# Optimization experiments

Hardware: AMD Instinct MI355X
Metric: run time of the kernel (lower is better)

## Reference

```python
import jax, jax.numpy as jnp
import numpy as np

EPS = 1e-4
GX, GY, ZMAX = 512, 512, 64
S0 = (GX, GY, ZMAX)

# ---------- rulebook construction (numpy, setup-time only) ----------

def _lin(c, S):
    return (c[:, 0].astype(np.int64) * S[1] + c[:, 1]) * S[2] + c[:, 2]

def _lookup(skeys, order, qk):
    pos = np.searchsorted(skeys, qk)
    pc = np.clip(pos, 0, len(skeys) - 1)
    ok = skeys[pc] == qk
    return np.where(ok, order[pc], -1).astype(np.int32)

def _sm_rulebook(coords, S):
    # submanifold 3x3x3: for each active site, index of neighbor at each of 27 offsets (-1 if inactive)
    keys = _lin(coords, S)
    order = np.argsort(keys).astype(np.int64); skeys = keys[order]
    Sa = np.array(S)
    cols = []
    for d in [(i, j, k) for i in (-1, 0, 1) for j in (-1, 0, 1) for k in (-1, 0, 1)]:
        q = coords + np.array(d)
        inb = np.all((q >= 0) & (q < Sa), axis=1)
        nb = _lookup(skeys, order, _lin(np.clip(q, 0, None), S))
        cols.append(np.where(inb, nb, -1).astype(np.int32))
    return np.stack(cols, 1)  # [N, 27]

def _down_rulebook(coords, S):
    # strided 2x2x2 conv: coarse sites = unique(coords//2); [Nc, 8] child indices into fine level
    Sc = (S[0] // 2, S[1] // 2, S[2] // 2)
    pk = np.unique(_lin(coords // 2, Sc))
    z = pk % Sc[2]; y = (pk // Sc[2]) % Sc[1]; x = pk // (Sc[1] * Sc[2])
    pcoords = np.stack([x, y, z], 1)
    keys = _lin(coords, S)
    order = np.argsort(keys).astype(np.int64); skeys = keys[order]
    cols = []
    for d in [(i, j, k) for i in (0, 1) for j in (0, 1) for k in (0, 1)]:
        cols.append(_lookup(skeys, order, _lin(pcoords * 2 + np.array(d), S)))
    return np.stack(cols, 1), pcoords, Sc

def _coords0():
    # road-like 2.5D surface: one active voxel per (x, y) column -> exactly 512*512 unique sites
    xs, ys = np.meshgrid(np.arange(GX), np.arange(GY), indexing='ij')
    x = xs.ravel().astype(np.int64); y = ys.ravel().astype(np.int64)
    z = (32 + 8 * np.sin(x / 37.0) + 8 * np.cos(y / 53.0) + 3 * np.sin((x + y) / 17.0)).astype(np.int64)
    z = np.clip(z, 0, ZMAX - 1)
    return np.stack([x, y, z], 1)


def setup_inputs() -> dict:
    c0 = _coords0()
    nbr_0 = _sm_rulebook(c0, S0)
    rb_0, c1, S1 = _down_rulebook(c0, S0)
    nbr_1 = _sm_rulebook(c1, S1)
    rb_1, c2, S2 = _down_rulebook(c1, S1)
    nbr_2 = _sm_rulebook(c2, S2)

    key = jax.random.key(0)
    ks = iter(jax.random.split(key, 40))
    def w(shape):
        fan = float(np.prod(shape[:-1]))
        return (jax.random.normal(next(ks), shape, jnp.float32) / np.sqrt(fan)).astype(jnp.float32)
    def gb(c):  # row 0 = gamma (~1), row 1 = beta (~0)
        base = jnp.concatenate([jnp.ones((1, c), jnp.float32), jnp.zeros((1, c), jnp.float32)], 0)
        return base + 0.01 * jax.random.normal(next(ks), (2, c), jnp.float32)

    N0 = c0.shape[0]
    return dict(
        feat=jax.random.normal(next(ks), (N0, 3), jnp.float32),
        w_in=w((27, 3, 32)),
        bn1_0=gb(32), w_sm1_0=w((27, 32, 32)),
        bnd_0=gb(32), w_down_0=w((8, 32, 64)),
        bn1_1=gb(64), w_sm1_1=w((27, 64, 64)),
        bnd_1=gb(64), w_down_1=w((8, 64, 96)),
        bn1_2=gb(96), w_sm1_2=w((27, 96, 96)),
        bnu_1=gb(96), w_up_1=w((8, 96, 64)),
        bn2_1=gb(128), w_sm2_1=w((27, 128, 64)),
        bnu_0=gb(64), w_up_0=w((8, 64, 32)),
        bn2_0=gb(64), w_sm2_0=w((27, 64, 32)),
        bnf=gb(32),
        lin_w=w((32, 2)), lin_b=jnp.zeros((2,), jnp.float32),
        nbr_0=jnp.asarray(nbr_0), nbr_1=jnp.asarray(nbr_1), nbr_2=jnp.asarray(nbr_2),
        rb_0=jnp.asarray(rb_0), rb_1=jnp.asarray(rb_1),
    )

# ---------- jax forward ----------

def bn_relu(x, gb):
    # SCN BatchNormReLU: normalize over all active sites (biased var), affine, then ReLU
    mu = jnp.mean(x, 0)
    var = jnp.var(x, 0)
    return jax.nn.relu((x - mu) * (gb[0] / jnp.sqrt(var + EPS)) + gb[1])

def sm_conv(feat, nbr, W):
    # submanifold conv: gather 27 neighbors (zero for inactive), per-offset GEMM, accumulate
    out = jnp.zeros((feat.shape[0], W.shape[2]), feat.dtype)
    for k in range(W.shape[0]):
        idx = nbr[:, k]
        g = jnp.where((idx >= 0)[:, None], feat[jnp.clip(idx, 0)], 0.0)
        out = out + g @ W[k]
    return out

def down_conv(feat, rb, W):
    # strided 2x2x2 conv: gather children of each coarse site
    out = jnp.zeros((rb.shape[0], W.shape[2]), feat.dtype)
    for k in range(W.shape[0]):
        idx = rb[:, k]
        g = jnp.where((idx >= 0)[:, None], feat[jnp.clip(idx, 0)], 0.0)
        out = out + g @ W[k]
    return out

def up_conv(feat_c, rb, W, n_fine):
    # deconv (transpose of down_conv): scatter coarse features back to fine active sites
    out = jnp.zeros((n_fine, W.shape[2]), feat_c.dtype)
    for k in range(W.shape[0]):
        idx = rb[:, k]
        contrib = jnp.where((idx >= 0)[:, None], feat_c @ W[k], 0.0)
        out = out.at[jnp.clip(idx, 0)].add(contrib)
    return out


def reference(feat, w_in, bn1_0, w_sm1_0, bnd_0, w_down_0, bn1_1, w_sm1_1, bnd_1, w_down_1,
              bn1_2, w_sm1_2, bnu_1, w_up_1, bn2_1, w_sm2_1, bnu_0, w_up_0, bn2_0, w_sm2_0,
              bnf, lin_w, lin_b, nbr_0, nbr_1, nbr_2, rb_0, rb_1):
    x0 = sm_conv(feat, nbr_0, w_in)                              # initial SMConv 3 -> 32
    x0 = sm_conv(bn_relu(x0, bn1_0), nbr_0, w_sm1_0)             # level-0 entry block
    d0 = down_conv(bn_relu(x0, bnd_0), rb_0, w_down_0)           # [N1, 64]
    x1 = sm_conv(bn_relu(d0, bn1_1), nbr_1, w_sm1_1)             # level-1 entry block
    d1 = down_conv(bn_relu(x1, bnd_1), rb_1, w_down_1)           # [N2, 96]
    x2 = sm_conv(bn_relu(d1, bn1_2), nbr_2, w_sm1_2)             # innermost block
    u1 = up_conv(bn_relu(x2, bnu_1), rb_1, w_up_1, x1.shape[0])  # deconv 96 -> 64
    y1 = sm_conv(bn_relu(jnp.concatenate([x1, u1], 1), bn2_1), nbr_1, w_sm2_1)  # 128 -> 64
    u0 = up_conv(bn_relu(y1, bnu_0), rb_0, w_up_0, x0.shape[0])  # deconv 64 -> 32
    y0 = sm_conv(bn_relu(jnp.concatenate([x0, u0], 1), bn2_0), nbr_0, w_sm2_0)  # 64 -> 32
    out = bn_relu(y0, bnf)                                       # final BatchNormReLU(m)
    return out @ lin_w + lin_b                                   # Linear(m, 2)
```

## Files before the change

### kernel.cpp

```cpp
#include <hip/hip_runtime.h>
#include <hip/hip_bf16.h>


typedef __hip_bfloat16 hbf;
typedef __attribute__((ext_vector_type(8))) short short8;
typedef __attribute__((ext_vector_type(4))) float f32x4;
typedef const __attribute__((address_space(1))) short gas_short;
typedef __attribute__((address_space(3))) short las_short;

__device__ inline float b2f(short s) {
    unsigned u = ((unsigned)(unsigned short)s) << 16;
    float f; __builtin_memcpy(&f, &u, 4); return f;
}
__device__ inline short f2b(float f) {
    hbf h = __float2bfloat16(f);
    short s; __builtin_memcpy(&s, &h, 2); return s;
}

struct WPA {
    const float* src[9];
    short* dst[9];
    int CI[9], CO[9];
    int cum[10];
};
__global__ __launch_bounds__(256) void wprep_all(WPA a, int total) {
    int e0 = blockIdx.x * 256 + threadIdx.x;
    if (e0 >= total) return;
    int L = 0;
#pragma unroll
    for (int i = 1; i < 9; i++) L += (e0 >= a.cum[i]) ? 1 : 0;
    int e = e0 - a.cum[L];
    int CI = a.CI[L], CO = a.CO[L];
    int NT = CO >> 4, NCH = CI >> 5;
    int j    = e & 7;
    int lane = (e >> 3) & 63;
    int t    = (e >> 9) % NT;
    int c    = (e / (512 * NT)) % NCH;
    int k    = e / (512 * NT * NCH);
    int ci = c * 32 + (lane >> 4) * 8 + j;
    int co = t * 16 + (lane & 15);
    a.dst[L][e] = f2b(a.src[L][((long long)k * CI + ci) * CO + co]);
}

__global__ void zerok(float* p, int n) {
    int i = blockIdx.x * 256 + threadIdx.x;
    if (i < n) p[i] = 0.f;
}

__global__ __launch_bounds__(256) void nbrmask_k(const int* __restrict__ nbr,
                                                 unsigned* __restrict__ msk, int N) {
    long long r = (long long)blockIdx.x * 256 + threadIdx.x;
    if (r >= N) return;
    unsigned mv = 0;
#pragma unroll
    for (int k = 0; k < 27; k++)
        mv |= (nbr[r * 27 + k] >= 0) ? (1u << k) : 0u;
    msk[r] = mv;
}

__global__ __launch_bounds__(256) void conv_in(
    const float* __restrict__ feat, const int* __restrict__ nbr,
    const float* __restrict__ W, short* __restrict__ out, int N) {
    __shared__ float sW[27 * 96];
    const int tid = threadIdx.x;
    for (int e = tid; e < 27 * 96; e += 256) sW[e] = W[e];
    __syncthreads();
    long long r = (long long)blockIdx.x * 256 + tid;
    if (r >= N) return;
    float acc[32];
#pragma unroll
    for (int c = 0; c < 32; c++) acc[c] = 0.f;
    for (int k = 0; k < 27; k++) {
        int idx = nbr[r * 27 + k];
        if (idx >= 0) {
            float f0 = feat[(long long)idx * 3];
            float f1 = feat[(long long)idx * 3 + 1];
            float f2 = feat[(long long)idx * 3 + 2];
            const float* w = sW + k * 96;
#pragma unroll
            for (int c = 0; c < 32; c++)
                acc[c] += f0 * w[c] + f1 * w[32 + c] + f2 * w[64 + c];
        }
    }
#pragma unroll
    for (int c = 0; c < 32; c++) out[r * 32 + c] = f2b(acc[c]);
}

template<int CI1, int CI2, int COUT>
__global__ __launch_bounds__(256) void stencil0(
    const short* __restrict__ fA, const short* __restrict__ fB,
    const unsigned* __restrict__ msk, const short* __restrict__ Wf,
    short* __restrict__ out, float* __restrict__ pstat,
    const float* __restrict__ abA, const float* __restrict__ abB, int N) {
    constexpr int CIT  = CI1 + CI2;
    constexpr int NCH  = CIT / 32;
    constexpr int NT   = COUT / 16;
    constexpr int MT   = 2;
    constexpr int CIB  = CIT * 2;
    constexpr int ROWS = 130;
    constexpr int NC8  = CIT / 8;
    constexpr int SWB  = (CIB >= 128) ? 7 : 3;
    __shared__ __attribute__((aligned(16))) char sA[3 * ROWS * CIB];
    const int tid  = threadIdx.x;
    const int lane = tid & 63;
    const int wid  = tid >> 6;
    const int m    = lane & 15;
    const int quad = lane >> 4;
    const int bid  = blockIdx.x;
    const int xq     = bid >> 2;
    const int ystart = (bid & 3) << 7;
    const long long R = (long long)bid * 128;

    {
        const int c8 = tid % NC8;
        const bool isA = (c8 * 8) < CI1;
        const short* src  = isA ? fA : fB;
        const float* abp  = isA ? abA : abB;
        const int   srcCI = isA ? CI1 : CI2;
        const int   chb   = isA ? c8 * 8 : c8 * 8 - CI1;
        float s_[8], b_[8];
#pragma unroll
        for (int jj = 0; jj < 8; jj++) {
            s_[jj] = abp[chb + jj];
            b_[jj] = abp[srcCI + chb + jj];
        }
        for (int e = tid; e < 3 * ROWS * NC8; e += 256) {
            int rr = (e / NC8) % ROWS;
            int st = e / (NC8 * ROWS);
            long long gr = (long long)(xq - 1 + st) * 512 + (ystart - 1 + rr);
            long long grc = (gr < 0 || gr >= N) ? 0 : gr;
            short8 v = *reinterpret_cast<const short8*>(src + grc * srcCI + chb);
            short8 o;
#pragma unroll
            for (int jj = 0; jj < 8; jj++) {
                float f = b2f(v[jj]) * s_[jj] + b_[jj];
                o[jj] = f2b(f > 0.f ? f : 0.f);
            }
            int byte = (st * ROWS + rr) * CIB + c8 * 16;
            byte ^= ((rr & SWB) << 4);
            *reinterpret_cast<short8*>(sA + byte) = o;
        }
    }
    __syncthreads();

    f32x4 acc[MT][NT];
#pragma unroll
    for (int mt = 0; mt < MT; mt++)
#pragma unroll
        for (int t = 0; t < NT; t++) acc[mt][t] = (f32x4)0.f;

    unsigned mv[MT];
#pragma unroll
    for (int mt = 0; mt < MT; mt++) {
        long long r = R + wid * 32 + mt * 16 + m;
        mv[mt] = (r < N) ? msk[r] : 0u;
    }

#pragma unroll
    for (int s9 = 0; s9 < 9; s9++) {
        const int st = s9 / 3;
        const int dy = s9 % 3 - 1;
        short8 a[MT][NCH];
#pragma unroll
        for (int mt = 0; mt < MT; mt++) {
            int rl = 1 + wid * 32 + mt * 16 + m + dy;
#pragma unroll
            for (int c = 0; c < NCH; c++) {
                int byte = (st * ROWS + rl) * CIB + (c * 4 + quad) * 16;
                byte ^= ((rl & SWB) << 4);
                a[mt][c] = *reinterpret_cast<const short8*>(sA + byte);
            }
        }
#pragma unroll
        for (int z3 = 0; z3 < 3; z3++) {
            const int k = s9 * 3 + z3;
            unsigned anyb = (mv[0] >> k) & 1;
            if (MT > 1) anyb |= (mv[1] >> k) & 1;
            if (__any(anyb)) {
                short8 bf[NCH][NT];
#pragma unroll
                for (int c = 0; c < NCH; c++)
#pragma unroll
                    for (int t = 0; t < NT; t++)
                        bf[c][t] = *reinterpret_cast<const short8*>(
                            Wf + ((size_t)(k * NCH + c) * NT + t) * 512 + lane * 8);
#pragma unroll
                for (int mt = 0; mt < MT; mt++) {
                    const bool bb = (mv[mt] >> k) & 1;
                    short8 asel[NCH];
#pragma unroll
                    for (int c = 0; c < NCH; c++)
                        asel[c] = bb ? a[mt][c] : (short8)0;
#pragma unroll
                    for (int c = 0; c < NCH; c++)
#pragma unroll
                        for (int t = 0; t < NT; t++)
                            acc[mt][t] = __builtin_amdgcn_mfma_f32_16x16x32_bf16(
                                asel[c], bf[c][t], acc[mt][t], 0, 0, 0);
                }
            }
        }
    }

    float s[NT], q[NT];
#pragma unroll
    for (int t = 0; t < NT; t++) { s[t] = 0.f; q[t] = 0.f; }
#pragma unroll
    for (int mt = 0; mt < MT; mt++) {
#pragma unroll
        for (int g4 = 0; g4 < 4; g4++) {
            long long sr = R + wid * 32 + mt * 16 + quad * 4 + g4;
            if (sr < N) {
#pragma unroll
                for (int t = 0; t < NT; t++) {
                    float v = acc[mt][t][g4];
                    out[sr * COUT + t * 16 + m] = f2b(v);
                    s[t] += v; q[t] += v * v;
                }
            }
        }
    }
    float* pb = pstat + (blockIdx.x & 7) * 2 * COUT;
#pragma unroll
    for (int t = 0; t < NT; t++) {
        float sv = s[t], qv = q[t];
        sv += __shfl_xor(sv, 16); qv += __shfl_xor(qv, 16);
        sv += __shfl_xor(sv, 32); qv += __shfl_xor(qv, 32);
        if (quad == 0) {
            atomicAdd(&pb[t * 16 + m], sv);
            atomicAdd(&pb[COUT + t * 16 + m], qv);
        }
    }
}

template<int CI1, int CI2, int COUT, int K, int G, int MT, bool FACT>
__global__ __launch_bounds__(256) void gmfma10(
    const short* __restrict__ fA, const short* __restrict__ fB,
    const int* __restrict__ nbr, const short* __restrict__ Wf,
    short* __restrict__ out, float* __restrict__ pstat,
    const float* __restrict__ abp, int N) {
    static_assert(K % G == 0, "G must divide K");
    static_assert(!FACT || CI2 == 0, "fused act only for single input");
    constexpr int NT  = COUT / 16;
    constexpr int NC1 = CI1 / 32;
    constexpr int NC2 = CI2 / 32;
    constexpr int NCH = (CI1 + CI2) / 32;
    constexpr int PANEL = NCH * NT * 512;
    constexpr int GSH   = G * PANEL;
    constexpr int NPH   = K / G;
    constexpr int WCH   = GSH / 4;
    constexpr int S16   = (WCH * 2) / 1024;
    constexpr int S4    = ((WCH * 2) % 1024) / 256;
    __shared__ __attribute__((aligned(16))) short sB[GSH];
    const int tid  = threadIdx.x;
    const int lane = tid & 63;
    const int wid  = tid >> 6;
    const int m    = lane & 15;
    const int quad = lane >> 4;
    const long long tb0 = ((long long)blockIdx.x * 4 + wid) * (MT * 16);

    f32x4 acc[MT][NT];
#pragma unroll
    for (int mt = 0; mt < MT; mt++)
#pragma unroll
        for (int t = 0; t < NT; t++) acc[mt][t] = (f32x4)0.f;

#define STAGE(ph)                                                              \
    {                                                                          \
        const short* _src = Wf + (size_t)(ph) * GSH + wid * WCH;               \
        short* _dst = &sB[wid * WCH];                                          \
        _Pragma("unroll")                                                      \
        for (int i = 0; i < S16; i++)                                          \
            __builtin_amdgcn_global_load_lds(                                  \
                (gas_short*)(_src + i * 512 + lane * 8),                       \
                (las_short*)(_dst + i * 512), 16, 0, 0);                       \
        _Pragma("unroll")                                                      \
        for (int i = 0; i < S4; i++)                                           \
            __builtin_amdgcn_global_load_lds(                                  \
                (gas_short*)(_src + S16 * 512 + i * 128 + lane * 2),           \
                (las_short*)(_dst + S16 * 512 + i * 128), 4, 0, 0);            \
    }

    STAGE(0)
    __builtin_amdgcn_sched_barrier(0);

    int idxs[MT][K];
#pragma unroll
    for (int mt = 0; mt < MT; mt++) {
        long long r = tb0 + mt * 16 + m;
        bool rv = r < N;
#pragma unroll
        for (int k = 0; k < K; k++)
            idxs[mt][k] = rv ? nbr[r * K + k] : -1;
    }
    unsigned pmask[MT];
#pragma unroll
    for (int mt = 0; mt < MT; mt++) {
        unsigned pm = 0;
#pragma unroll
        for (int k = 0; k < K; k++)
            pm |= __any(idxs[mt][k] >= 0) ? (1u << k) : 0u;
        pmask[mt] = __builtin_amdgcn_readfirstlane(pm);
    }

    float aS[FACT ? NC1 * 8 : 1], aBb[FACT ? NC1 * 8 : 1];
    if constexpr (FACT) {
#pragma unroll
        for (int c = 0; c < NC1; c++)
#pragma unroll
            for (int jj = 0; jj < 8; jj++) {
                int ch = c * 32 + quad * 8 + jj;
                aS[c * 8 + jj]  = abp[ch];
                aBb[c * 8 + jj] = abp[CI1 + ch];
            }
    }

    __builtin_amdgcn_sched_barrier(0);
    asm volatile("s_waitcnt vmcnt(0)" ::: "memory");
    __builtin_amdgcn_s_barrier();
    __builtin_amdgcn_sched_barrier(0);
    asm volatile("" ::: "memory");

    short8 S[3][NCH];

#define LOADS(sl, mt, kk)                                                      \
    {                                                                          \
        int _i = idxs[mt][kk];                                                 \
        long long _j = _i < 0 ? 0 : _i;                                        \
        _Pragma("unroll")                                                      \
        for (int c = 0; c < NC1; c++) {                                        \
            short8 _v = *reinterpret_cast<const short8*>(                      \
                fA + _j * CI1 + c * 32 + quad * 8);                            \
            if constexpr (FACT) {                                              \
                short8 _o;                                                     \
                _Pragma("unroll")                                              \
                for (int jj = 0; jj < 8; jj++) {                               \
                    float _f = b2f(_v[jj]) * aS[c * 8 + jj] + aBb[c * 8 + jj]; \
                    _o[jj] = f2b(_f > 0.f ? _f : 0.f);                         \
                }                                                              \
                _v = _o;                                                       \
            }                                                                  \
            S[sl][c] = (_i >= 0) ? _v : (short8)0;                             \
        }                                                                      \
        if constexpr (NC2 > 0) {                                               \
            _Pragma("unroll")                                                  \
            for (int c = 0; c < NC2; c++) {                                    \
                short8 _v = *reinterpret_cast<const short8*>(                  \
                    fB + _j * CI2 + c * 32 + quad * 8);                        \
                S[sl][NC1 + c] = (_i >= 0) ? _v : (short8)0;                   \
            }                                                                  \
        }                                                                      \
    }
#define MFMAS(sl, mt, jl)                                                      \
    {                                                                          \
        _Pragma("unroll")                                                      \
        for (int c = 0; c < NCH; c++) {                                        \
            _Pragma("unroll")                                                  \
            for (int t = 0; t < NT; t++) {                                     \
                short8 b = *reinterpret_cast<const short8*>(                   \
                    &sB[((jl) * NCH * NT + c * NT + t) * 512 + lane * 8]);     \
                acc[mt][t] = __builtin_amdgcn_mfma_f32_16x16x32_bf16(          \
                    S[sl][c], b, acc[mt][t], 0, 0, 0);                         \
            }                                                                  \
        }                                                                      \
    }

#pragma unroll
    for (int ph = 0; ph < NPH; ph++) {
#pragma unroll
        for (int mt = 0; mt < MT; mt++) {
            const unsigned mm = (pmask[mt] >> (ph * G)) & ((1u << G) - 1);
#pragma unroll
            for (int j = 0; j < G + 2; j++) {
                if (j < G)
                    if (mm & (1u << j)) LOADS(j % 3, mt, ph * G + j)
                if (j >= 2)
                    if (mm & (1u << (j - 2))) MFMAS((j - 2) % 3, mt, j - 2)
            }
        }
        if (ph + 1 < NPH) {
            __builtin_amdgcn_sched_barrier(0);
            asm volatile("s_waitcnt lgkmcnt(0)" ::: "memory");
            __builtin_amdgcn_s_barrier();
            __builtin_amdgcn_sched_barrier(0);
            STAGE(ph + 1)
            __builtin_amdgcn_sched_barrier(0);
            asm volatile("s_waitcnt vmcnt(0)" ::: "memory");
            __builtin_amdgcn_s_barrier();
            __builtin_amdgcn_sched_barrier(0);
            asm volatile("" ::: "memory");
        }
    }
#undef LOADS
#undef MFMAS
#undef STAGE
    float s[NT], q[NT];
#pragma unroll
    for (int t = 0; t < NT; t++) { s[t] = 0.f; q[t] = 0.f; }
#pragma unroll
    for (int mt = 0; mt < MT; mt++) {
#pragma unroll
        for (int g4 = 0; g4 < 4; g4++) {
            long long sr = tb0 + mt * 16 + quad * 4 + g4;
            if (sr < N) {
#pragma unroll
                for (int t = 0; t < NT; t++) {
                    float v = acc[mt][t][g4];
                    out[sr * COUT + t * 16 + m] = f2b(v);
                    s[t] += v; q[t] += v * v;
                }
            }
        }
    }
    float* pb = pstat + (blockIdx.x & 7) * 2 * COUT;
#pragma unroll
    for (int t = 0; t < NT; t++) {
        float sv = s[t], qv = q[t];
        sv += __shfl_xor(sv, 16); qv += __shfl_xor(qv, 16);
        sv += __shfl_xor(sv, 32); qv += __shfl_xor(qv, 32);
        if (quad == 0) {
            atomicAdd(&pb[t * 16 + m], sv);
            atomicAdd(&pb[COUT + t * 16 + m], qv);
        }
    }
}

template<int CIN, int COUT, int G>
__global__ __launch_bounds__(256) void upmfma10(
    const short* __restrict__ f, const int* __restrict__ rb,
    const short* __restrict__ Wf, short* __restrict__ out,
    float* __restrict__ pstat, const float* __restrict__ abp, int N) {
    static_assert(8 % G == 0, "G must divide 8");
    constexpr int NT = COUT / 16;
    constexpr int NK = CIN / 32;
    constexpr int PANEL = NK * NT * 512;
    constexpr int GSH   = G * PANEL;
    constexpr int NPH   = 8 / G;
    constexpr int WCH   = GSH / 4;
    constexpr int S16   = (WCH * 2) / 1024;
    constexpr int S4    = ((WCH * 2) % 1024) / 256;
    __shared__ __attribute__((aligned(16))) short sB[GSH];
    const int tid  = threadIdx.x;
    const int lane = tid & 63;
    const int wid  = tid >> 6;
    const int m    = lane & 15;
    const int quad = lane >> 4;
    const long long row0 = ((long long)blockIdx.x * 4 + wid) * 16;
    const long long r = row0 + m;
    const bool rv = r < N;
    const long long rc = rv ? r : 0;

#define STAGE(ph)                                                              \
    {                                                                          \
        const short* _src = Wf + (size_t)(ph) * GSH + wid * WCH;               \
        short* _dst = &sB[wid * WCH];                                          \
        _Pragma("unroll")                                                      \
        for (int i = 0; i < S16; i++)                                          \
            __builtin_amdgcn_global_load_lds(                                  \
                (gas_short*)(_src + i * 512 + lane * 8),                       \
                (las_short*)(_dst + i * 512), 16, 0, 0);                       \
        _Pragma("unroll")                                                      \
        for (int i = 0; i < S4; i++)                                           \
            __builtin_amdgcn_global_load_lds(                                  \
                (gas_short*)(_src + S16 * 512 + i * 128 + lane * 2),           \
                (las_short*)(_dst + S16 * 512 + i * 128), 4, 0, 0);            \
    }
    STAGE(0)
    __builtin_amdgcn_sched_barrier(0);

    short8 af[NK];
#pragma unroll
    for (int kc = 0; kc < NK; kc++) {
        short8 v = *reinterpret_cast<const short8*>(
            f + rc * CIN + kc * 32 + quad * 8);
        short8 o;
#pragma unroll
        for (int jj = 0; jj < 8; jj++) {
            int ch = kc * 32 + quad * 8 + jj;
            float u = b2f(v[jj]) * abp[ch] + abp[CIN + ch];
            o[jj] = f2b(u > 0.f ? u : 0.f);
        }
        af[kc] = rv ? o : (short8)0;
    }
    int sidx[8][4];
#pragma unroll
    for (int g4 = 0; g4 < 4; g4++) {
        long long sr = row0 + quad * 4 + g4;
#pragma unroll
        for (int k = 0; k < 8; k++)
            sidx[k][g4] = (sr < N) ? rb[sr * 8 + k] : -1;
    }
    unsigned pm = 0;
#pragma unroll
    for (int k = 0; k < 8; k++) {
        int anyv = (sidx[k][0] >= 0) | (sidx[k][1] >= 0) |
                   (sidx[k][2] >= 0) | (sidx[k][3] >= 0);
        pm |= __any(anyv) ? (1u << k) : 0u;
    }
    pm = __builtin_amdgcn_readfirstlane(pm);

    float s[NT], q[NT];
#pragma unroll
    for (int t = 0; t < NT; t++) { s[t] = 0.f; q[t] = 0.f; }

    __builtin_amdgcn_sched_barrier(0);
    asm volatile("s_waitcnt vmcnt(0)" ::: "memory");
    __builtin_amdgcn_s_barrier();
    __builtin_amdgcn_sched_barrier(0);
    asm volatile("" ::: "memory");

#pragma unroll
    for (int ph = 0; ph < NPH; ph++) {
#pragma unroll
        for (int j = 0; j < G; j++) {
            const int k = ph * G + j;
            if (pm & (1u << k)) {
                f32x4 acc[NT];
#pragma unroll
                for (int t = 0; t < NT; t++) acc[t] = (f32x4)0.f;
#pragma unroll
                for (int kc = 0; kc < NK; kc++) {
#pragma unroll
                    for (int t = 0; t < NT; t++) {
                        short8 b = *reinterpret_cast<const short8*>(
                            &sB[(j * NK * NT + kc * NT + t) * 512 + lane * 8]);
                        acc[t] = __builtin_amdgcn_mfma_f32_16x16x32_bf16(
                            af[kc], b, acc[t], 0, 0, 0);
                    }
                }
#pragma unroll
                for (int g4 = 0; g4 < 4; g4++) {
                    if (sidx[k][g4] >= 0) {
#pragma unroll
                        for (int t = 0; t < NT; t++) {
                            float v = acc[t][g4];
                            out[(long long)sidx[k][g4] * COUT + t * 16 + m] =
                                f2b(v);
                            s[t] += v; q[t] += v * v;
                        }
                    }
                }
            }
        }
        if (ph + 1 < NPH) {
            __builtin_amdgcn_sched_barrier(0);
            asm volatile("s_waitcnt lgkmcnt(0)" ::: "memory");
            __builtin_amdgcn_s_barrier();
            __builtin_amdgcn_sched_barrier(0);
            STAGE(ph + 1)
            __builtin_amdgcn_sched_barrier(0);
            asm volatile("s_waitcnt vmcnt(0)" ::: "memory");
            __builtin_amdgcn_s_barrier();
            __builtin_amdgcn_sched_barrier(0);
            asm volatile("" ::: "memory");
        }
    }
#undef STAGE
    float* pb = pstat + (blockIdx.x & 7) * 2 * COUT;
#pragma unroll
    for (int t = 0; t < NT; t++) {
        float sv = s[t], qv = q[t];
        sv += __shfl_xor(sv, 16); qv += __shfl_xor(qv, 16);
        sv += __shfl_xor(sv, 32); qv += __shfl_xor(qv, 32);
        if (quad == 0) {
            atomicAdd(&pb[t * 16 + m], sv);
            atomicAdd(&pb[COUT + t * 16 + m], qv);
        }
    }
}

template<int C>
__global__ void bn_stats(const short* __restrict__ x, double* __restrict__ part, int N) {
    constexpr int GR  = C / 8;
    constexpr int RPB = 256 / GR;
    constexpr int ACTIVE = GR * RPB;
    __shared__ double ls[256 * 8];
    __shared__ double lq[256 * 8];
    const int tid = threadIdx.x;
    const int g   = tid % GR;
    const int rr  = tid / GR;
    double s[8], q[8];
#pragma unroll
    for (int j = 0; j < 8; j++) { s[j] = 0.0; q[j] = 0.0; }
    if (tid < ACTIVE) {
        for (long long r = (long long)blockIdx.x * RPB + rr; r < N;
             r += (long long)gridDim.x * RPB) {
            short8 v = *reinterpret_cast<const short8*>(x + r * C + g * 8);
#pragma unroll
            for (int j = 0; j < 8; j++) {
                double f = (double)b2f(v[j]);
                s[j] += f; q[j] += f * f;
            }
        }
    }
#pragma unroll
    for (int j = 0; j < 8; j++) { ls[tid * 8 + j] = s[j]; lq[tid * 8 + j] = q[j]; }
    __syncthreads();
    if (tid < C) {
        int gg = tid / 8, jj = tid % 8;
        double S = 0.0, Q = 0.0;
        for (int r2 = 0; r2 < RPB; r2++) {
            S += ls[(r2 * GR + gg) * 8 + jj];
            Q += lq[(r2 * GR + gg) * 8 + jj];
        }
        part[blockIdx.x * 256 + tid]       = S;
        part[blockIdx.x * 256 + 128 + tid] = Q;
    }
}

__global__ void bn_fin(const double* __restrict__ part, const float* __restrict__ gb,
                       int gbfull, int goff, float* __restrict__ ab,
                       int C, int P, double invN) {
    __shared__ double ss[256], sq[256];
    const int tid = threadIdx.x;
    const int c   = tid % C;
    const int g   = tid / C;
    const int G   = 256 / C;
    double s = 0.0, q = 0.0;
    if (g < G) {
        for (int p = g; p < P; p += G) {
            s += part[p * 256 + c];
            q += part[p * 256 + 128 + c];
        }
    }
    ss[tid] = s; sq[tid] = q;
    __syncthreads();
    if (tid < C) {
        for (int j = 1; j < G; j++) { s += ss[j * C + c]; q += sq[j * C + c]; }
        double mu  = s * invN;
        double var = q * invN - mu * mu;
        double a   = (double)gb[goff + c] / sqrt(var + 1e-4);
        ab[c]     = (float)a;
        ab[C + c] = (float)((double)gb[gbfull + goff + c] - mu * a);
    }
}

__global__ void bn_fin_a(const float* __restrict__ pst, const float* __restrict__ gb,
                         int gbfull, int goff, float* __restrict__ ab,
                         int C, double invN) {
    int c = threadIdx.x;
    if (c >= C) return;
    double s = 0.0, q = 0.0;
#pragma unroll
    for (int b = 0; b < 8; b++) {
        s += (double)pst[b * 2 * C + c];
        q += (double)pst[b * 2 * C + C + c];
    }
    double mu  = s * invN;
    double var = q * invN - mu * mu;
    double a   = (double)gb[goff + c] / sqrt(var + 1e-4);
    ab[c]     = (float)a;
    ab[C + c] = (float)((double)gb[gbfull + goff + c] - mu * a);
}

template<int C>
__global__ void bnact(const short* __restrict__ x, const float* __restrict__ ab,
                      short* __restrict__ y, long long total8) {
    long long i = (long long)blockIdx.x * blockDim.x + threadIdx.x;
    if (i >= total8) return;
    long long base = i * 8;
    int c0 = (int)(base % C);
    short8 v = *reinterpret_cast<const short8*>(x + base);
    short8 o;
#pragma unroll
    for (int j = 0; j < 8; j++) {
        float f = b2f(v[j]) * ab[c0 + j] + ab[C + c0 + j];
        o[j] = f2b(f > 0.f ? f : 0.f);
    }
    *reinterpret_cast<short8*>(y + base) = o;
}

template<int C>
__global__ void bnact2(const short* __restrict__ xa, const float* __restrict__ aba,
                       short* __restrict__ ya,
                       const short* __restrict__ xb, const float* __restrict__ abb,
                       short* __restrict__ yb, long long n8) {
    long long i = (long long)blockIdx.x * blockDim.x + threadIdx.x;
    if (i >= 2 * n8) return;
    const short* x; const float* ab; short* y; long long ii;
    if (i < n8) { x = xa; ab = aba; y = ya; ii = i; }
    else        { x = xb; ab = abb; y = yb; ii = i - n8; }
    long long base = ii * 8;
    int c0 = (int)(base % C);
    short8 v = *reinterpret_cast<const short8*>(x + base);
    short8 o;
#pragma unroll
    for (int j = 0; j < 8; j++) {
        float f = b2f(v[j]) * ab[c0 + j] + ab[C + c0 + j];
        o[j] = f2b(f > 0.f ? f : 0.f);
    }
    *reinterpret_cast<short8*>(y + base) = o;
}

__global__ void final_k(const short* __restrict__ x, const float* __restrict__ ab,
                        const float* __restrict__ lw, const float* __restrict__ lb,
                        float* __restrict__ out, int N) {
    long long r = (long long)blockIdx.x * blockDim.x + threadIdx.x;
    if (r >= N) return;
    float a0 = lb[0], a1 = lb[1];
#pragma unroll
    for (int j = 0; j < 4; j++) {
        short8 v = *reinterpret_cast<const short8*>(x + r * 32 + j * 8);
#pragma unroll
        for (int t = 0; t < 8; t++) {
            int ci = 8 * j + t;
            float u = b2f(v[t]) * ab[ci] + ab[32 + ci];
            u = u > 0.f ? u : 0.f;
            a0 += u * lw[ci * 2];
            a1 += u * lw[ci * 2 + 1];
        }
    }
    out[2 * r]     = a0;
    out[2 * r + 1] = a1;
}

extern "C" void kernel_launch(void* const* d_in, const int* in_sizes, int n_in,
                              void* d_out, int out_size, void* d_ws, size_t ws_size,
                              hipStream_t stream) {
    const long long N0 = in_sizes[0] / 3;
    const long long N1 = in_sizes[26] / 8;
    const long long N2 = in_sizes[27] / 8;
    const int P = 256;

    const float* feat = (const float*)d_in[0];
    const int* nbr0 = (const int*)d_in[23];
    const int* nbr1 = (const int*)d_in[24];
    const int* nbr2 = (const int*)d_in[25];
    const int* rb0  = (const int*)d_in[26];
    const int* rb1  = (const int*)d_in[27];

    char* p = (char*)d_ws;
    double* part = (double*)p;            p += (size_t)P * 256 * 8;
    float*  ab   = (float*)p;             p += 12 * 256 * 4;
    float*  pst  = (float*)p;             p += (size_t)10 * 2048 * 4;
    unsigned* msk0 = (unsigned*)p;        p += ((size_t)N0 * 4 + 63) & ~(size_t)63;
    const int wLayer[9] = {3, 5, 7, 9, 11, 13, 15, 17, 19};
    const int wK[9]  = {27, 8, 27, 8, 27, 8, 27, 8, 27};
    const int wCI[9] = {32, 32, 64, 64, 96, 96, 128, 64, 64};
    const int wCO[9] = {32, 64, 64, 96, 96, 64, 64, 32, 32};
    short* wt[9];
    WPA wpa;
    int cum = 0;
    for (int i = 0; i < 9; i++) {
        wt[i] = (short*)p;
        int n = wK[i] * wCI[i] * wCO[i];
        p += (((size_t)n * 2 + 63) & ~(size_t)63);
        wpa.src[i] = (const float*)d_in[wLayer[i]];
        wpa.dst[i] = wt[i];
        wpa.CI[i] = wCI[i]; wpa.CO[i] = wCO[i];
        wpa.cum[i] = cum; cum += n;
    }
    wpa.cum[9] = cum;
    auto balloc = [&](long long elems) {
        short* q = (short*)p;
        p += (((size_t)elems * 2 + 63) & ~(size_t)63);
        return q;
    };
    short* R0 = balloc(N0 * 32);
    short* R1 = balloc(N0 * 32);
    short* R2 = balloc(N1 * 64);
    short* R3 = balloc(N0 * 32);
    short* Xb = balloc(N0 * 32);
    short* Yb = balloc(N0 * 32);

    wprep_all<<<(cum + 255) / 256, 256, 0, stream>>>(wpa, cum);
    zerok<<<(10 * 2048 + 255) / 256, 256, 0, stream>>>(pst, 10 * 2048);
    nbrmask_k<<<(int)((N0 + 255) / 256), 256, 0, stream>>>(nbr0, msk0, (int)N0);

#define AB(SL) (ab + (SL) * 256)
#define PS(SL) (pst + (SL) * 2048)
#define FINA(PSL, GBI, GBFULL, GOFF, SL, CH, NN)                                     \
    bn_fin_a<<<1, 128, 0, stream>>>(PS(PSL), (const float*)d_in[GBI], GBFULL, GOFF,  \
                                    AB(SL), CH, 1.0 / (double)(NN))
#define GB1(N_) (int)(((N_) + 63) / 64)
#define GB2(N_) (int)(((N_) + 127) / 128)

    conv_in<<<(int)((N0 + 255) / 256), 256, 0, stream>>>(
        feat, nbr0, (const float*)d_in[1], R0, (int)N0);
    bn_stats<32><<<P, 256, 0, stream>>>(R0, part, (int)N0);
    bn_fin<<<1, 256, 0, stream>>>(part, (const float*)d_in[2], 32, 0,
                                  AB(0), 32, P, 1.0 / (double)N0);
    stencil0<32, 0, 32><<<GB2(N0), 256, 0, stream>>>(
        R0, nullptr, msk0, wt[0], R1, PS(0), AB(0), nullptr, (int)N0);
    FINA(0, 4, 32, 0, 1, 32, N0);
    FINA(0, 18, 64, 0, 9, 32, N0);
    gmfma10<32, 0, 64, 8, 8, 2, true><<<GB2(N1), 256, 0, stream>>>(
        R1, nullptr, rb0, wt[1], R0, PS(1), AB(1), (int)N1);
    FINA(1, 6, 64, 0, 2, 64, N1);

    bnact<64><<<(int)((N1 * 64 / 8 + 255) / 256), 256, 0, stream>>>(
        R0, AB(2), Xb, N1 * 64 / 8);
    gmfma10<64, 0, 64, 27, 3, 2, false><<<GB2(N1), 256, 0, stream>>>(
        Xb, nullptr, nbr1, wt[2], R2, PS(2), nullptr, (int)N1);
    FINA(2, 8, 64, 0, 3, 64, N1);
    FINA(2, 14, 128, 0, 6, 64, N1);
    gmfma10<64, 0, 96, 8, 2, 1, true><<<GB1(N2), 256, 0, stream>>>(
        R2, nullptr, rb1, wt[3], R0, PS(3), AB(3), (int)N2);
    FINA(3, 10, 96, 0, 4, 96, N2);

    bnact<96><<<(int)((N2 * 96 / 8 + 255) / 256), 256, 0, stream>>>(
        R0, AB(4), Xb, N2 * 96 / 8);
    gmfma10<96, 0, 96, 27, 3, 1, false><<<GB1(N2), 256, 0, stream>>>(
        Xb, nullptr, nbr2, wt[4], R3, PS(4), nullptr, (int)N2);
    FINA(4, 12, 96, 0, 5, 96, N2);

    upmfma10<96, 64, 2><<<GB1(N2), 256, 0, stream>>>(
        R3, rb1, wt[5], R0, PS(5), AB(5), (int)N2);
    FINA(5, 14, 128, 64, 7, 64, N1);
    bnact2<64><<<(int)((2 * (N1 * 64 / 8) + 255) / 256), 256, 0, stream>>>(
        R2, AB(6), Xb, R0, AB(7), Yb, N1 * 64 / 8);
    gmfma10<64, 64, 64, 27, 3, 2, false><<<GB2(N1), 256, 0, stream>>>(
        Xb, Yb, nbr1, wt[6], R3, PS(6), nullptr, (int)N1);
    FINA(6, 16, 64, 0, 8, 64, N1);

    upmfma10<64, 32, 4><<<GB1(N1), 256, 0, stream>>>(
        R3, rb0, wt[7], R0, PS(7), AB(8), (int)N1);
    FINA(7, 18, 64, 32, 10, 32, N0);
    stencil0<32, 32, 32><<<GB2(N0), 256, 0, stream>>>(
        R1, R0, msk0, wt[8], R3, PS(8), AB(9), AB(10), (int)N0);
    FINA(8, 20, 32, 0, 11, 32, N0);

    final_k<<<(int)((N0 + 255) / 256), 256, 0, stream>>>(
        R3, AB(11), (const float*)d_in[21], (const float*)d_in[22],
        (float*)d_out, (int)N0);

#undef AB
#undef PS
#undef FINA
#undef GB1
#undef GB2
}
```

Before: 566.0 us.

## Read MFMA weight fragments directly from global memory instead of staging in LDS

The gathered-conv and up-conv MFMA kernels no longer stage weight panels into shared memory with async global-to-LDS loads and phase barriers. Each wave now loads its B fragments straight from global memory (relying on L1/L2 caching), and the phased loop becomes a single software-pipelined loop over all kernel offsets. This removes LDS usage, block-wide barriers and phase synchronisation, which may raise occupancy. The cost is redundant per-wave global/cache traffic for the weights and exposed load latency before each MFMA.

After: 681.5 us. 1.2x slower.

```diff
diff --git a/kernel.cpp b/kernel.cpp
--- a/kernel.cpp
+++ b/kernel.cpp
@@ -5,8 +5,6 @@
 typedef __hip_bfloat16 hbf;
 typedef __attribute__((ext_vector_type(8))) short short8;
 typedef __attribute__((ext_vector_type(4))) float f32x4;
-typedef const __attribute__((address_space(1))) short gas_short;
-typedef __attribute__((address_space(3))) short las_short;
 
 __device__ inline float b2f(short s) {
     unsigned u = ((unsigned)(unsigned short)s) << 16;
@@ -233,25 +231,17 @@
     }
 }
 
-template<int CI1, int CI2, int COUT, int K, int G, int MT, bool FACT>
-__global__ __launch_bounds__(256) void gmfma10(
+template<int CI1, int CI2, int COUT, int K, int MT, bool FACT>
+__global__ __launch_bounds__(256) void gmfma11(
     const short* __restrict__ fA, const short* __restrict__ fB,
     const int* __restrict__ nbr, const short* __restrict__ Wf,
     short* __restrict__ out, float* __restrict__ pstat,
     const float* __restrict__ abp, int N) {
-    static_assert(K % G == 0, "G must divide K");
     static_assert(!FACT || CI2 == 0, "fused act only for single input");
     constexpr int NT  = COUT / 16;
     constexpr int NC1 = CI1 / 32;
     constexpr int NC2 = CI2 / 32;
     constexpr int NCH = (CI1 + CI2) / 32;
-    constexpr int PANEL = NCH * NT * 512;
-    constexpr int GSH   = G * PANEL;
-    constexpr int NPH   = K / G;
-    constexpr int WCH   = GSH / 4;
-    constexpr int S16   = (WCH * 2) / 1024;
-    constexpr int S4    = ((WCH * 2) % 1024) / 256;
-    __shared__ __attribute__((aligned(16))) short sB[GSH];
     const int tid  = threadIdx.x;
     const int lane = tid & 63;
     const int wid  = tid >> 6;
@@ -265,25 +255,6 @@
 #pragma unroll
         for (int t = 0; t < NT; t++) acc[mt][t] = (f32x4)0.f;
 
-#define STAGE(ph)                                                              \
-    {                                                                          \
-        const short* _src = Wf + (size_t)(ph) * GSH + wid * WCH;               \
-        short* _dst = &sB[wid * WCH];                                          \
-        _Pragma("unroll")                                                      \
-        for (int i = 0; i < S16; i++)                                          \
-            __builtin_amdgcn_global_load_lds(                                  \
-                (gas_short*)(_src + i * 512 + lane * 8),                       \
-                (las_short*)(_dst + i * 512), 16, 0, 0);                       \
-        _Pragma("unroll")                                                      \
-        for (int i = 0; i < S4; i++)                                           \
-            __builtin_amdgcn_global_load_lds(                                  \
-                (gas_short*)(_src + S16 * 512 + i * 128 + lane * 2),           \
-                (las_short*)(_dst + S16 * 512 + i * 128), 4, 0, 0);            \
-    }
-
-    STAGE(0)
-    __builtin_amdgcn_sched_barrier(0);
-
     int idxs[MT][K];
 #pragma unroll
     for (int mt = 0; mt < MT; mt++) {
@@ -314,12 +285,6 @@
                 aBb[c * 8 + jj] = abp[CI1 + ch];
             }
     }
-
-    __builtin_amdgcn_sched_barrier(0);
-    asm volatile("s_waitcnt vmcnt(0)" ::: "memory");
-    __builtin_amdgcn_s_barrier();
-    __builtin_amdgcn_sched_barrier(0);
-    asm volatile("" ::: "memory");
 
     short8 S[3][NCH];
 
@@ -351,14 +316,14 @@
             }                                                                  \
         }                                                                      \
     }
-#define MFMAS(sl, mt, jl)                                                      \
+#define MFMAD(sl, mt, kk)                                                      \
     {                                                                          \
         _Pragma("unroll")                                                      \
         for (int c = 0; c < NCH; c++) {                                        \
             _Pragma("unroll")                                                  \
             for (int t = 0; t < NT; t++) {                                     \
                 short8 b = *reinterpret_cast<const short8*>(                   \
-                    &sB[((jl) * NCH * NT + c * NT + t) * 512 + lane * 8]);     \
+                    Wf + ((size_t)((kk) * NCH + c) * NT + t) * 512 + lane * 8);\
                 acc[mt][t] = __builtin_amdgcn_mfma_f32_16x16x32_bf16(          \
                     S[sl][c], b, acc[mt][t], 0, 0, 0);                         \
             }                                                                  \
@@ -366,34 +331,19 @@
     }
 
 #pragma unroll
-    for (int ph = 0; ph < NPH; ph++) {
-#pragma unroll
-        for (int mt = 0; mt < MT; mt++) {
-            const unsigned mm = (pmask[mt] >> (ph * G)) & ((1u << G) - 1);
-#pragma unroll
-            for (int j = 0; j < G + 2; j++) {
-                if (j < G)
-                    if (mm & (1u << j)) LOADS(j % 3, mt, ph * G + j)
-                if (j >= 2)
-                    if (mm & (1u << (j - 2))) MFMAS((j - 2) % 3, mt, j - 2)
-            }
-        }
-        if (ph + 1 < NPH) {
-            __builtin_amdgcn_sched_barrier(0);
-            asm volatile("s_waitcnt lgkmcnt(0)" ::: "memory");
-            __builtin_amdgcn_s_barrier();
-            __builtin_amdgcn_sched_barrier(0);
-            STAGE(ph + 1)
-            __builtin_amdgcn_sched_barrier(0);
-            asm volatile("s_waitcnt vmcnt(0)" ::: "memory");
-            __builtin_amdgcn_s_barrier();
-            __builtin_amdgcn_sched_barrier(0);
-            asm volatile("" ::: "memory");
+    for (int mt = 0; mt < MT; mt++) {
+        const unsigned mm = pmask[mt];
+        if (mm & 1u) LOADS(0, mt, 0)
+        if (K > 1 && (mm & 2u)) LOADS(1, mt, 1)
+#pragma unroll
+        for (int k = 0; k < K; k++) {
+            if (k + 2 < K)
+                if (mm & (1u << (k + 2))) LOADS((k + 2) % 3, mt, k + 2)
+            if (mm & (1u << k)) MFMAD(k % 3, mt, k)
         }
     }
 #undef LOADS
-#undef MFMAS
-#undef STAGE
+#undef MFMAD
     float s[NT], q[NT];
 #pragma unroll
     for (int t = 0; t < NT; t++) { s[t] = 0.f; q[t] = 0.f; }
@@ -425,21 +375,13 @@
     }
 }
 
-template<int CIN, int COUT, int G>
-__global__ __launch_bounds__(256) void upmfma10(
+template<int CIN, int COUT>
+__global__ __launch_bounds__(256) void upmfma11(
     const short* __restrict__ f, const int* __restrict__ rb,
     const short* __restrict__ Wf, short* __restrict__ out,
     float* __restrict__ pstat, const float* __restrict__ abp, int N) {
-    static_assert(8 % G == 0, "G must divide 8");
     constexpr int NT = COUT / 16;
     constexpr int NK = CIN / 32;
-    constexpr int PANEL = NK * NT * 512;
-    constexpr int GSH   = G * PANEL;
-    constexpr int NPH   = 8 / G;
-    constexpr int WCH   = GSH / 4;
-    constexpr int S16   = (WCH * 2) / 1024;
-    constexpr int S4    = ((WCH * 2) % 1024) / 256;
-    __shared__ __attribute__((aligned(16))) short sB[GSH];
     const int tid  = threadIdx.x;
     const int lane = tid & 63;
     const int wid  = tid >> 6;
@@ -450,24 +392,6 @@
     const bool rv = r < N;
     const long long rc = rv ? r : 0;
 
-#define STAGE(ph)                                                              \
-    {                                                                          \
-        const short* _src = Wf + (size_t)(ph) * GSH + wid * WCH;               \
-        short* _dst = &sB[wid * WCH];                                          \
-        _Pragma("unroll")                                                      \
-        for (int i = 0; i < S16; i++)                                          \
-            __builtin_amdgcn_global_load_lds(                                  \
-                (gas_short*)(_src + i * 512 + lane * 8),                       \
-                (las_short*)(_dst + i * 512), 16, 0, 0);                       \
-        _Pragma("unroll")                                                      \
-        for (int i = 0; i < S4; i++)                                           \
-            __builtin_amdgcn_global_load_lds(                                  \
-                (gas_short*)(_src + S16 * 512 + i * 128 + lane * 2),           \
-                (las_short*)(_dst + S16 * 512 + i * 128), 4, 0, 0);            \
-    }
-    STAGE(0)
-    __builtin_amdgcn_sched_barrier(0);
-
     short8 af[NK];
 #pragma unroll
     for (int kc = 0; kc < NK; kc++) {
@@ -503,59 +427,35 @@
 #pragma unroll
     for (int t = 0; t < NT; t++) { s[t] = 0.f; q[t] = 0.f; }
 
-    __builtin_amdgcn_sched_barrier(0);
-    asm volatile("s_waitcnt vmcnt(0)" ::: "memory");
-    __builtin_amdgcn_s_barrier();
-    __builtin_amdgcn_sched_barrier(0);
-    asm volatile("" ::: "memory");
-
-#pragma unroll
-    for (int ph = 0; ph < NPH; ph++) {
-#pragma unroll
-        for (int j = 0; j < G; j++) {
-            const int k = ph * G + j;
-            if (pm & (1u << k)) {
-                f32x4 acc[NT];
-#pragma unroll
-                for (int t = 0; t < NT; t++) acc[t] = (f32x4)0.f;
-#pragma unroll
-                for (int kc = 0; kc < NK; kc++) {
+#pragma unroll
+    for (int k = 0; k < 8; k++) {
+        if (pm & (1u << k)) {
+            f32x4 acc[NT];
+#pragma unroll
+            for (int t = 0; t < NT; t++) acc[t] = (f32x4)0.f;
+#pragma unroll
+            for (int kc = 0; kc < NK; kc++) {
+#pragma unroll
+                for (int t = 0; t < NT; t++) {
+                    short8 b = *reinterpret_cast<const short8*>(
+                        Wf + ((size_t)(k * NK + kc) * NT + t) * 512 + lane * 8);
+                    acc[t] = __builtin_amdgcn_mfma_f32_16x16x32_bf16(
+                        af[kc], b, acc[t], 0, 0, 0);
+                }
+            }
+#pragma unroll
+            for (int g4 = 0; g4 < 4; g4++) {
+                if (sidx[k][g4] >= 0) {
 #pragma unroll
                     for (int t = 0; t < NT; t++) {
-                        short8 b = *reinterpret_cast<const short8*>(
-                            &sB[(j * NK * NT + kc * NT + t) * 512 + lane * 8]);
-                        acc[t] = __builtin_amdgcn_mfma_f32_16x16x32_bf16(
-                            af[kc], b, acc[t], 0, 0, 0);
+                        float v = acc[t][g4];
+                        out[(long long)sidx[k][g4] * COUT + t * 16 + m] = f2b(v);
+                        s[t] += v; q[t] += v * v;
                     }
                 }
-#pragma unroll
-                for (int g4 = 0; g4 < 4; g4++) {
-                    if (sidx[k][g4] >= 0) {
-#pragma unroll
-                        for (int t = 0; t < NT; t++) {
-                            float v = acc[t][g4];
-                            out[(long long)sidx[k][g4] * COUT + t * 16 + m] =
-                                f2b(v);
-                            s[t] += v; q[t] += v * v;
-                        }
-                    }
-                }
-            }
-        }
-        if (ph + 1 < NPH) {
-            __builtin_amdgcn_sched_barrier(0);
-            asm volatile("s_waitcnt lgkmcnt(0)" ::: "memory");
-            __builtin_amdgcn_s_barrier();
-            __builtin_amdgcn_sched_barrier(0);
-            STAGE(ph + 1)
-            __builtin_amdgcn_sched_barrier(0);
-            asm volatile("s_waitcnt vmcnt(0)" ::: "memory");
-            __builtin_amdgcn_s_barrier();
-            __builtin_amdgcn_sched_barrier(0);
-            asm volatile("" ::: "memory");
-        }
-    }
-#undef STAGE
+            }
+        }
+    }
     float* pb = pstat + (blockIdx.x & 7) * 2 * COUT;
 #pragma unroll
     for (int t = 0; t < NT; t++) {
@@ -784,36 +684,36 @@
         R0, nullptr, msk0, wt[0], R1, PS(0), AB(0), nullptr, (int)N0);
     FINA(0, 4, 32, 0, 1, 32, N0);
     FINA(0, 18, 64, 0, 9, 32, N0);
-    gmfma10<32, 0, 64, 8, 8, 2, true><<<GB2(N1), 256, 0, stream>>>(
+    gmfma11<32, 0, 64, 8, 2, true><<<GB2(N1), 256, 0, stream>>>(
         R1, nullptr, rb0, wt[1], R0, PS(1), AB(1), (int)N1);
     FINA(1, 6, 64, 0, 2, 64, N1);
 
     bnact<64><<<(int)((N1 * 64 / 8 + 255) / 256), 256, 0, stream>>>(
         R0, AB(2), Xb, N1 * 64 / 8);
-    gmfma10<64, 0, 64, 27, 3, 2, false><<<GB2(N1), 256, 0, stream>>>(
+    gmfma11<64, 0, 64, 27, 2, false><<<GB2(N1), 256, 0, stream>>>(
         Xb, nullptr, nbr1, wt[2], R2, PS(2), nullptr, (int)N1);
     FINA(2, 8, 64, 0, 3, 64, N1);
     FINA(2, 14, 128, 0, 6, 64, N1);
-    gmfma10<64, 0, 96, 8, 2, 1, true><<<GB1(N2), 256, 0, stream>>>(
+    gmfma11<64, 0, 96, 8, 1, true><<<GB1(N2), 256, 0, stream>>>(
         R2, nullptr, rb1, wt[3], R0, PS(3), AB(3), (int)N2);
     FINA(3, 10, 96, 0, 4, 96, N2);
 
     bnact<96><<<(int)((N2 * 96 / 8 + 255) / 256), 256, 0, stream>>>(
         R0, AB(4), Xb, N2 * 96 / 8);
-    gmfma10<96, 0, 96, 27, 3, 1, false><<<GB1(N2), 256, 0, stream>>>(
+    gmfma11<96, 0, 96, 27, 1, false><<<GB1(N2), 256, 0, stream>>>(
         Xb, nullptr, nbr2, wt[4], R3, PS(4), nullptr, (int)N2);
     FINA(4, 12, 96, 0, 5, 96, N2);
 
-    upmfma10<96, 64, 2><<<GB1(N2), 256, 0, stream>>>(
+    upmfma11<96, 64><<<GB1(N2), 256, 0, stream>>>(
         R3, rb1, wt[5], R0, PS(5), AB(5), (int)N2);
     FINA(5, 14, 128, 64, 7, 64, N1);
     bnact2<64><<<(int)((2 * (N1 * 64 / 8) + 255) / 256), 256, 0, stream>>>(
         R2, AB(6), Xb, R0, AB(7), Yb, N1 * 64 / 8);
-    gmfma10<64, 64, 64, 27, 3, 2, false><<<GB2(N1), 256, 0, stream>>>(
+    gmfma11<64, 64, 64, 27, 2, false><<<GB2(N1), 256, 0, stream>>>(
         Xb, Yb, nbr1, wt[6], R3, PS(6), nullptr, (int)N1);
     FINA(6, 16, 64, 0, 8, 64, N1);
 
-    upmfma10<64, 32, 4><<<GB1(N1), 256, 0, stream>>>(
+    upmfma11<64, 32><<<GB1(N1), 256, 0, stream>>>(
         R3, rb0, wt[7], R0, PS(7), AB(8), (int)N1);
     FINA(7, 18, 64, 32, 10, 32, N0);
     stencil0<32, 32, 32><<<GB2(N0), 256, 0, stream>>>(
```

## Split submanifold conv kernel offsets across waves with LDS reduction

Applied to the files above, without the earlier changes.

Adds a gksp kernel that splits the 27 kernel offsets across the 4 waves of a block. Each wave accumulates its share of offsets with MFMA for a smaller row tile, skips offsets that are empty for the whole wave, and the partial results are reduced through shared memory before the bf16 store and BN statistics. The three level-1 and level-2 submanifold convs now use it. Blocks cover fewer rows, so there are many more blocks, giving more parallelism on the small coarse levels. In exchange it adds an LDS reduction and a barrier per block, and each weight panel is reused across fewer rows.

Measured after the change: 616.0 us. 8.8% more time.

```diff
diff --git a/kernel.cpp b/kernel.cpp
--- a/kernel.cpp
+++ b/kernel.cpp
@@ -230,6 +230,151 @@
             atomicAdd(&pb[t * 16 + m], sv);
             atomicAdd(&pb[COUT + t * 16 + m], qv);
         }
+    }
+}
+
+template<int CI1, int CI2, int COUT, int K, int MT>
+__global__ __launch_bounds__(256) void gksp(
+    const short* __restrict__ fA, const short* __restrict__ fB,
+    const int* __restrict__ nbr, const short* __restrict__ Wf,
+    short* __restrict__ out, float* __restrict__ pstat, int N) {
+    constexpr int NT  = COUT / 16;
+    constexpr int NC1 = CI1 / 32;
+    constexpr int NC2 = CI2 / 32;
+    constexpr int NCH = (CI1 + CI2) / 32;
+    constexpr int CHK = (K + 3) / 4;
+    constexpr int RPB = MT * 16;
+    __shared__ float sR[4][RPB][COUT];
+    const int tid  = threadIdx.x;
+    const int lane = tid & 63;
+    const int wid  = tid >> 6;
+    const int m    = lane & 15;
+    const int quad = lane >> 4;
+    const long long R = (long long)blockIdx.x * RPB;
+
+    const int base = K / 4, rem = K % 4;
+    const int clen = base + (wid < rem ? 1 : 0);
+    const int k0   = wid * base + (wid < rem ? wid : rem);
+
+    f32x4 acc[MT][NT];
+#pragma unroll
+    for (int mt = 0; mt < MT; mt++)
+#pragma unroll
+        for (int t = 0; t < NT; t++) acc[mt][t] = (f32x4)0.f;
+
+    int idxs[MT][CHK];
+#pragma unroll
+    for (int mt = 0; mt < MT; mt++) {
+        long long r = R + mt * 16 + m;
+        bool rv = r < N;
+#pragma unroll
+        for (int kk = 0; kk < CHK; kk++)
+            idxs[mt][kk] = (rv && kk < clen) ? nbr[r * K + k0 + kk] : -1;
+    }
+    unsigned pmask[MT];
+#pragma unroll
+    for (int mt = 0; mt < MT; mt++) {
+        unsigned pm = 0;
+#pragma unroll
+        for (int kk = 0; kk < CHK; kk++)
+            pm |= __any(idxs[mt][kk] >= 0) ? (1u << kk) : 0u;
+        pmask[mt] = __builtin_amdgcn_readfirstlane(pm);
+    }
+
+    short8 S[3][NCH];
+
+#define LOADS(sl, mt, kk)                                                      \
+    {                                                                          \
+        int _i = idxs[mt][kk];                                                 \
+        long long _j = _i < 0 ? 0 : _i;                                        \
+        _Pragma("unroll")                                                      \
+        for (int c = 0; c < NC1; c++) {                                        \
+            short8 _v = *reinterpret_cast<const short8*>(                      \
+                fA + _j * CI1 + c * 32 + quad * 8);                            \
+            S[sl][c] = (_i >= 0) ? _v : (short8)0;                             \
+        }                                                                      \
+        if constexpr (NC2 > 0) {                                               \
+            _Pragma("unroll")                                                  \
+            for (int c = 0; c < NC2; c++) {                                    \
+                short8 _v = *reinterpret_cast<const short8*>(                  \
+                    fB + _j * CI2 + c * 32 + quad * 8);                        \
+                S[sl][NC1 + c] = (_i >= 0) ? _v : (short8)0;                   \
+            }                                                                  \
+        }                                                                      \
+    }
+#define MFMAD(sl, mt, kk)                                                      \
+    {                                                                          \
+        _Pragma("unroll")                                                      \
+        for (int c = 0; c < NCH; c++) {                                        \
+            _Pragma("unroll")                                                  \
+            for (int t = 0; t < NT; t++) {                                     \
+                short8 b = *reinterpret_cast<const short8*>(                   \
+                    Wf + ((size_t)((k0 + (kk)) * NCH + c) * NT + t) * 512 +    \
+                    lane * 8);                                                 \
+                acc[mt][t] = __builtin_amdgcn_mfma_f32_16x16x32_bf16(          \
+                    S[sl][c], b, acc[mt][t], 0, 0, 0);                         \
+            }                                                                  \
+        }                                                                      \
+    }
+
+#pragma unroll
+    for (int mt = 0; mt < MT; mt++) {
+        const unsigned mm = pmask[mt];
+        if (mm & 1u) LOADS(0, mt, 0)
+        if (CHK > 1 && (mm & 2u)) LOADS(1, mt, 1)
+#pragma unroll
+        for (int kk = 0; kk < CHK; kk++) {
+            if (kk + 2 < CHK)
+                if (mm & (1u << (kk + 2))) LOADS((kk + 2) % 3, mt, kk + 2)
+            if (mm & (1u << kk)) MFMAD(kk % 3, mt, kk)
+        }
+    }
+#undef LOADS
+#undef MFMAD
+
+#pragma unroll
+    for (int mt = 0; mt < MT; mt++)
+#pragma unroll
+        for (int t = 0; t < NT; t++)
+#pragma unroll
+            for (int g4 = 0; g4 < 4; g4++)
+                sR[wid][mt * 16 + quad * 4 + g4][t * 16 + m] = acc[mt][t][g4];
+    __syncthreads();
+
+    constexpr int CH8 = COUT / 8;
+    {
+        const int row = tid / CH8;
+        const int ch0 = (tid % CH8) * 8;
+        if (row < RPB) {
+            long long sr = R + row;
+            float val[8];
+#pragma unroll
+            for (int j = 0; j < 8; j++)
+                val[j] = ((sR[0][row][ch0 + j] + sR[1][row][ch0 + j]) +
+                          (sR[2][row][ch0 + j] + sR[3][row][ch0 + j]));
+            if (sr < N) {
+                short8 o;
+#pragma unroll
+                for (int j = 0; j < 8; j++) o[j] = f2b(val[j]);
+                *reinterpret_cast<short8*>(out + sr * COUT + ch0) = o;
+            }
+#pragma unroll
+            for (int j = 0; j < 8; j++)
+                sR[0][row][ch0 + j] = (sr < N) ? val[j] : 0.f;
+        }
+    }
+    __syncthreads();
+
+    if (tid < COUT) {
+        float Sv = 0.f, Qv = 0.f;
+#pragma unroll
+        for (int row = 0; row < RPB; row++) {
+            float v = sR[0][row][tid];
+            Sv += v; Qv += v * v;
+        }
+        float* pb = pstat + (blockIdx.x & 7) * 2 * COUT;
+        atomicAdd(&pb[tid], Sv);
+        atomicAdd(&pb[COUT + tid], Qv);
     }
 }
 
@@ -774,6 +919,8 @@
                                     AB(SL), CH, 1.0 / (double)(NN))
 #define GB1(N_) (int)(((N_) + 63) / 64)
 #define GB2(N_) (int)(((N_) + 127) / 128)
+#define GK2(N_) (int)(((N_) + 31) / 32)
+#define GK1(N_) (int)(((N_) + 15) / 16)
 
     conv_in<<<(int)((N0 + 255) / 256), 256, 0, stream>>>(
         feat, nbr0, (const float*)d_in[1], R0, (int)N0);
@@ -790,8 +937,8 @@
 
     bnact<64><<<(int)((N1 * 64 / 8 + 255) / 256), 256, 0, stream>>>(
         R0, AB(2), Xb, N1 * 64 / 8);
-    gmfma10<64, 0, 64, 27, 3, 2, false><<<GB2(N1), 256, 0, stream>>>(
-        Xb, nullptr, nbr1, wt[2], R2, PS(2), nullptr, (int)N1);
+    gksp<64, 0, 64, 27, 2><<<GK2(N1), 256, 0, stream>>>(
+        Xb, nullptr, nbr1, wt[2], R2, PS(2), (int)N1);
     FINA(2, 8, 64, 0, 3, 64, N1);
     FINA(2, 14, 128, 0, 6, 64, N1);
     gmfma10<64, 0, 96, 8, 2, 1, true><<<GB1(N2), 256, 0, stream>>>(
@@ -800,8 +947,8 @@
 
     bnact<96><<<(int)((N2 * 96 / 8 + 255) / 256), 256, 0, stream>>>(
         R0, AB(4), Xb, N2 * 96 / 8);
-    gmfma10<96, 0, 96, 27, 3, 1, false><<<GB1(N2), 256, 0, stream>>>(
-        Xb, nullptr, nbr2, wt[4], R3, PS(4), nullptr, (int)N2);
+    gksp<96, 0, 96, 27, 1><<<GK1(N2), 256, 0, stream>>>(
+        Xb, nullptr, nbr2, wt[4], R3, PS(4), (int)N2);
     FINA(4, 12, 96, 0, 5, 96, N2);
 
     upmfma10<96, 64, 2><<<GB1(N2), 256, 0, stream>>>(
@@ -809,8 +956,8 @@
     FINA(5, 14, 128, 64, 7, 64, N1);
     bnact2<64><<<(int)((2 * (N1 * 64 / 8) + 255) / 256), 256, 0, stream>>>(
         R2, AB(6), Xb, R0, AB(7), Yb, N1 * 64 / 8);
-    gmfma10<64, 64, 64, 27, 3, 2, false><<<GB2(N1), 256, 0, stream>>>(
-        Xb, Yb, nbr1, wt[6], R3, PS(6), nullptr, (int)N1);
+    gksp<64, 64, 64, 27, 2><<<GK2(N1), 256, 0, stream>>>(
+        Xb, Yb, nbr1, wt[6], R3, PS(6), (int)N1);
     FINA(6, 16, 64, 0, 8, 64, N1);
 
     upmfma10<64, 32, 4><<<GB1(N1), 256, 0, stream>>>(
@@ -829,4 +976,6 @@
 #undef FINA
 #undef GB1
 #undef GB2
-}
+#undef GK2
+#undef GK1
+}
```
